# Kernel optimization log

Measured on AMD Instinct MI355X. Metric: run time of the kernel, lower is better.

Reference implementation:

```python
import jax, jax.numpy as jnp
import numpy as np

B, C_LOCAL, C_GUIDE, C2, H, W = 16, 256, 256, 256, 64, 64
MID = C2 // 2          # mlp hidden channels
CQ = C_LOCAL // 4      # offset_gen hidden channels (also = groups)
EPS = 1e-5             # BatchNorm eps (inference mode)


def _conv(x, w, pad=0, groups=1, b=None):
    out = jax.lax.conv_general_dilated(
        x, w, window_strides=(1, 1), padding=((pad, pad), (pad, pad)),
        dimension_numbers=('NCHW', 'OIHW', 'NCHW'), feature_group_count=groups)
    if b is not None:
        out = out + b[None, :, None, None]
    return out


def _bn(x, g, b, m, v):
    scale = g / jnp.sqrt(v + EPS)
    return x * scale[None, :, None, None] + (b - m * scale)[None, :, None, None]


def _grid_sample(img, grid):
    # img: [C,H,W]; grid: [H,W,2] with (x,y) in [-1,1]; bilinear, zeros padding,
    # align_corners=False (pixel = ((g+1)*size - 1)/2)
    C, Hh, Ww = img.shape
    ix = (grid[..., 0] + 1.0) * (Ww * 0.5) - 0.5
    iy = (grid[..., 1] + 1.0) * (Hh * 0.5) - 0.5
    x0 = jnp.floor(ix); y0 = jnp.floor(iy)
    x1 = x0 + 1.0;      y1 = y0 + 1.0
    wx1 = ix - x0; wx0 = 1.0 - wx1
    wy1 = iy - y0; wy0 = 1.0 - wy1

    def gather(xi, yi):
        valid = (xi >= 0) & (xi < Ww) & (yi >= 0) & (yi < Hh)
        xc = jnp.clip(xi, 0, Ww - 1).astype(jnp.int32)
        yc = jnp.clip(yi, 0, Hh - 1).astype(jnp.int32)
        return img[:, yc, xc] * valid.astype(img.dtype)[None]  # [C,H,W]

    return (gather(x0, y0) * (wx0 * wy0)[None]
            + gather(x1, y0) * (wx1 * wy0)[None]
            + gather(x0, y1) * (wx0 * wy1)[None]
            + gather(x1, y1) * (wx1 * wy1)[None])


def setup_inputs() -> dict:
    key = jax.random.key(0)
    ks = jax.random.split(key, 20)
    w = lambda k, s: jax.random.normal(k, s, jnp.float32) * 0.05
    return {
        'x_local': jax.random.normal(ks[0], (B, C_LOCAL, H, W), jnp.float32),
        'x_guide': jax.random.normal(ks[1], (B, C_GUIDE, H, W), jnp.float32),
        'w_align': w(ks[2], (C2, C_GUIDE, 1, 1)),
        'bn1_g': 1.0 + 0.1 * jax.random.normal(ks[3], (C2,), jnp.float32),
        'bn1_b': 0.1 * jax.random.normal(ks[4], (C2,), jnp.float32),
        'bn1_m': 0.1 * jax.random.normal(ks[5], (C2,), jnp.float32),
        'bn1_v': 0.5 + jax.random.uniform(ks[6], (C2,), jnp.float32),
        'w_off1': w(ks[7], (CQ, 4, 3, 3)),   # grouped: in-ch per group = C_LOCAL/CQ = 4
        'w_off2': w(ks[8], (2, CQ, 1, 1)),
        'b_off2': 0.1 * jax.random.normal(ks[9], (2,), jnp.float32),
        'w_mlp1': w(ks[10], (MID, C_LOCAL, 1, 1)),
        'bn2_g': 1.0 + 0.1 * jax.random.normal(ks[11], (MID,), jnp.float32),
        'bn2_b': 0.1 * jax.random.normal(ks[12], (MID,), jnp.float32),
        'bn2_m': 0.1 * jax.random.normal(ks[13], (MID,), jnp.float32),
        'bn2_v': 0.5 + jax.random.uniform(ks[14], (MID,), jnp.float32),
        'w_mlp2': w(ks[15], (C2, MID, 1, 1)),
    }


def reference(x_local, x_guide, w_align, bn1_g, bn1_b, bn1_m, bn1_v,
              w_off1, w_off2, b_off2, w_mlp1, bn2_g, bn2_b, bn2_m, bn2_v,
              w_mlp2):
    # align(x_guide): 1x1 conv + BN
    g = _bn(_conv(x_guide, w_align), bn1_g, bn1_b, bn1_m, bn1_v)
    # offset_gen(x_local): grouped 3x3 conv -> SiLU -> 1x1 conv (bias) -> [B,2,H,W]
    off = _conv(x_local, w_off1, pad=1, groups=CQ)
    off = _conv(jax.nn.silu(off), w_off2, b=b_off2)
    # base grid in [-1,1], (x,y) last
    ys = jnp.linspace(-1.0, 1.0, H)
    xs = jnp.linspace(-1.0, 1.0, W)
    gy, gx = jnp.meshgrid(ys, xs, indexing='ij')
    base = jnp.stack((gx, gy), axis=-1)                      # [H,W,2]
    v_grid = base[None] + off.transpose(0, 2, 3, 1) * (2.0 / max(H, W))
    g_aligned = jax.vmap(_grid_sample)(g, v_grid)            # [B,C2,H,W]
    # mlp(x_local): 1x1 conv -> BN -> GELU(exact) -> 1x1 conv
    l = _conv(x_local, w_mlp1)
    l = jax.nn.gelu(_bn(l, bn2_g, bn2_b, bn2_m, bn2_v), approximate=False)
    l = _conv(l, w_mlp2)
    return jax.nn.silu(g_aligned + l)
```

## Files before the change

### kernel.cpp

```cpp
#include <hip/hip_runtime.h>

typedef unsigned short u16;
typedef unsigned int u32;
typedef __bf16 bf16x8 __attribute__((ext_vector_type(8)));
typedef float f32x4 __attribute__((ext_vector_type(4)));
typedef u16 u16x4 __attribute__((ext_vector_type(4)));
typedef u16 u16x8 __attribute__((ext_vector_type(8)));

#define EPS 1e-5f

__device__ __forceinline__ u16 f2bf(float f) {
  unsigned u = __builtin_bit_cast(unsigned, f);
  u += 0x7FFFu + ((u >> 16) & 1u);
  return (u16)(u >> 16);
}
__device__ __forceinline__ float bf2f(u16 h) {
  unsigned u = ((unsigned)h) << 16;
  return __builtin_bit_cast(float, u);
}

__global__ void prep_weights(
    const float* __restrict__ wa, const float* __restrict__ g1, const float* __restrict__ b1,
    const float* __restrict__ m1, const float* __restrict__ v1,
    const float* __restrict__ w1, const float* __restrict__ g2, const float* __restrict__ b2,
    const float* __restrict__ m2, const float* __restrict__ v2,
    const float* __restrict__ w2,
    u16* __restrict__ Acat, u16* __restrict__ w1_o,
    float* __restrict__ bias1, float* __restrict__ bias2) {
  int c = blockIdx.x, k = threadIdx.x;
  float s1 = g1[c] / sqrtf(v1[c] + EPS);
  if (k < 256) Acat[c * 384 + k] = f2bf(wa[c * 256 + k] * s1);
  else         Acat[c * 384 + k] = f2bf(w2[c * 128 + (k - 256)]);
  if (c < 128) {
    float s2 = g2[c] / sqrtf(v2[c] + EPS);
    if (k < 256) w1_o[c * 256 + k] = f2bf(w1[c * 256 + k] * s2);
    if (k == 256) bias2[c] = b2[c] - m2[c] * s2;
  }
  if (k == 0) bias1[c] = b1[c] - m1[c] * s1;
}

__global__ __launch_bounds__(256) void gconv_kernel(
    const float* __restrict__ xl, const float* __restrict__ w1,
    u16* __restrict__ sbuf) {
  __shared__ float tile[4][18][68];
  const int tid = threadIdx.x;
  const int band = blockIdx.x;
  const int q = blockIdx.y;
  const int b = blockIdx.z;
  const float* xb = xl + ((size_t)b * 256 + 4 * q) * 4096;

  if (tid < 72) {
    int ci0 = tid / 18, r0_ = tid - ci0 * 18;
    float* rowp = &tile[ci0][r0_][0];
    rowp[0] = 0.f; rowp[65] = 0.f; rowp[66] = 0.f; rowp[67] = 0.f;
  }

  const int ci = tid >> 6, col = tid & 63;
  const int gy0 = band * 16 - 1;
  const float* cp = xb + (size_t)ci * 4096 + col;
  float v[18];
#pragma unroll
  for (int r = 0; r < 18; ++r) {
    int gy = gy0 + r;
    int gyc = min(max(gy, 0), 63);
    float raw = cp[gyc * 64];
    v[r] = ((unsigned)gy < 64u) ? raw : 0.f;
  }
#pragma unroll
  for (int r = 0; r < 18; ++r) tile[ci][r][col + 1] = v[r];

  float wq[36];
#pragma unroll
  for (int i = 0; i < 36; ++i) wq[i] = w1[q * 36 + i];
  __syncthreads();

  const int qx = tid & 15, ry = tid >> 4;
  float a0 = 0.f, a1 = 0.f, a2 = 0.f, a3 = 0.f;
#pragma unroll
  for (int ci2 = 0; ci2 < 4; ++ci2) {
#pragma unroll
    for (int dy = 0; dy < 3; ++dy) {
      const float* rowp = &tile[ci2][ry + dy][qx * 4];
      f32x4 m = *(const f32x4*)rowp;
      float2 e = *(const float2*)(rowp + 4);
      float w0 = wq[ci2 * 9 + dy * 3 + 0];
      float w1_ = wq[ci2 * 9 + dy * 3 + 1];
      float w2_ = wq[ci2 * 9 + dy * 3 + 2];
      a0 += w0 * m[0] + w1_ * m[1] + w2_ * m[2];
      a1 += w0 * m[1] + w1_ * m[2] + w2_ * m[3];
      a2 += w0 * m[2] + w1_ * m[3] + w2_ * e.x;
      a3 += w0 * m[3] + w1_ * e.x  + w2_ * e.y;
    }
  }
  u16x4 o;
  o[0] = f2bf(a0 / (1.f + __expf(-a0)));
  o[1] = f2bf(a1 / (1.f + __expf(-a1)));
  o[2] = f2bf(a2 / (1.f + __expf(-a2)));
  o[3] = f2bf(a3 / (1.f + __expf(-a3)));
  u16* sp = sbuf + ((size_t)(b * 64 + q)) * 4096 + (band * 16 + ry) * 64 + qx * 4;
  *(u16x4*)sp = o;
}

__global__ __launch_bounds__(256) void coords_kernel(
    const u16* __restrict__ sbuf, const float* __restrict__ w2,
    const float* __restrict__ b2, float* __restrict__ coords,
    float* __restrict__ wsum) {
  __shared__ float sw2[128];
  const int tid = threadIdx.x;
  if (tid < 128) sw2[tid] = w2[tid];
  __syncthreads();
  const int b = blockIdx.y;
  const int p = blockIdx.x * 256 + tid;
  const u16* sp = sbuf + (size_t)b * 64 * 4096 + p;
  float ax = 0.f, ay = 0.f;
#pragma unroll 8
  for (int q = 0; q < 64; ++q) {
    float v = bf2f(sp[(size_t)q * 4096]);
    ax += sw2[q] * v;
    ay += sw2[64 + q] * v;
  }
  int y = p >> 6, x = p & 63;
  float ix = (64.f / 63.f) * (float)x + ax + b2[0] - 0.5f;
  float iy = (64.f / 63.f) * (float)y + ay + b2[1] - 0.5f;
  ((float2*)coords)[(size_t)b * 4096 + p] = make_float2(ix, iy);
  float x0f = floorf(ix), y0f = floorf(iy);
  int x0 = (int)x0f, y0 = (int)y0f;
  float wx1 = ix - x0f, wx0 = 1.f - wx1;
  float wy1 = iy - y0f, wy0 = 1.f - wy1;
  bool vx0 = (unsigned)x0 < 64u, vx1 = (unsigned)(x0 + 1) < 64u;
  bool vy0 = (unsigned)y0 < 64u, vy1 = (unsigned)(y0 + 1) < 64u;
  float s = (vx0 && vy0 ? wx0 * wy0 : 0.f) + (vx1 && vy0 ? wx1 * wy0 : 0.f) +
            (vx0 && vy1 ? wx0 * wy1 : 0.f) + (vx1 && vy1 ? wx1 * wy1 : 0.f);
  wsum[(size_t)b * 4096 + p] = s;
}

__global__ __launch_bounds__(256, 1) void sampler_kernel(
    const float* __restrict__ xg, const float* __restrict__ coords,
    u16* __restrict__ xh) {
  __shared__ u16 t[64 * 72];
  const int wg = blockIdx.x;
  const int id = (wg & 7) * 512 + (wg >> 3);
  const int kq = id >> 10;
  const int b = (id >> 6) & 15, row = id & 63;
  const int tid = threadIdx.x;
  const int px = tid & 63, ko = tid >> 6;
  const int p = row * 64 + px;
  float2 cd = ((const float2*)coords)[(size_t)b * 4096 + p];
  float ix = cd.x, iy = cd.y;
  float x0f = floorf(ix), y0f = floorf(iy);
  int x0 = (int)x0f, y0 = (int)y0f;
  float wx1 = ix - x0f, wx0 = 1.f - wx1;
  float wy1 = iy - y0f, wy0 = 1.f - wy1;
  bool vx0 = (unsigned)x0 < 64u, vx1 = (unsigned)(x0 + 1) < 64u;
  bool vy0 = (unsigned)y0 < 64u, vy1 = (unsigned)(y0 + 1) < 64u;
  int x0c = min(max(x0, 0), 63), x1c = min(max(x0 + 1, 0), 63);
  int y0c = min(max(y0, 0), 63), y1c = min(max(y0 + 1, 0), 63);
  float w00 = (vx0 && vy0) ? wx0 * wy0 : 0.f;
  float w10 = (vx1 && vy0) ? wx1 * wy0 : 0.f;
  float w01 = (vx0 && vy1) ? wx0 * wy1 : 0.f;
  float w11 = (vx1 && vy1) ? wx1 * wy1 : 0.f;
  const int i00 = y0c * 64 + x0c, i10 = y0c * 64 + x1c;
  const int i01 = y1c * 64 + x0c, i11 = y1c * 64 + x1c;
  const float* bb = xg + ((size_t)b * 256 + kq * 64 + ko * 16) * 4096;

  float v00[16], v10[16], v01[16], v11[16];
#pragma unroll
  for (int kk = 0; kk < 16; ++kk) {
    const float* bp = bb + (size_t)kk * 4096;
    v00[kk] = bp[i00];
    v10[kk] = bp[i10];
    v01[kk] = bp[i01];
    v11[kk] = bp[i11];
  }
  u16 o[16];
#pragma unroll
  for (int kk = 0; kk < 16; ++kk) {
    float v = w00 * v00[kk] + w10 * v10[kk] + w01 * v01[kk] + w11 * v11[kk];
    o[kk] = f2bf(v);
  }
  *(u16x8*)&t[px * 72 + ko * 16] = *(u16x8*)&o[0];
  *(u16x8*)&t[px * 72 + ko * 16 + 8] = *(u16x8*)&o[8];
  __syncthreads();
  const int seg = tid & 7, pxa = tid >> 3;
  u16* base = xh + ((size_t)b * 4096 + row * 64) * 384 + kq * 64 + seg * 8;
#pragma unroll
  for (int h = 0; h < 2; ++h) {
    int pp = pxa + h * 32;
    *(u16x8*)(base + (size_t)pp * 384) = *(const u16x8*)&t[pp * 72 + seg * 8];
  }
}

__global__ __launch_bounds__(256, 2) void gemm_h(
    const u16* __restrict__ A, const float* __restrict__ Bsrc,
    u16* __restrict__ xh, const float* __restrict__ bias) {
  __shared__ u16 Al[2][128][40];
  __shared__ u16 Bl[2][128][40];
  const int tid = threadIdx.x;
  const int b = blockIdx.y;
  const int n0 = blockIdx.x * 128;
  const int wave = tid >> 6, lane = tid & 63;
  const int wr = wave >> 1, wc = wave & 1;
  const int lr = lane & 15, kg = lane >> 4;
  f32x4 acc[4][4] = {};
  const float* Bf = Bsrc + (size_t)b * 256 * 4096;

  const int am = tid >> 1, apos = (tid & 1) * 16;
  const int nq = tid & 31, kq = tid >> 5;
  const int nb = n0 + nq * 4;

  u16x8 qa0, qa1;
  f32x4 qb[4];
  {
    qa0 = *(const u16x8*)(A + (size_t)am * 256 + 0 + apos);
    qa1 = *(const u16x8*)(A + (size_t)am * 256 + 0 + apos + 8);
#pragma unroll
    for (int i = 0; i < 4; ++i)
      qb[i] = *(const f32x4*)(Bf + (size_t)(kq * 4 + i) * 4096 + nb);
  }
  int cur = 0;
  for (int kt = 0; kt < 8; ++kt) {
    *(u16x8*)&Al[cur][am][apos] = qa0;
    *(u16x8*)&Al[cur][am][apos + 8] = qa1;
#pragma unroll
    for (int j = 0; j < 4; ++j) {
      u16x4 w = {f2bf(qb[0][j]), f2bf(qb[1][j]), f2bf(qb[2][j]), f2bf(qb[3][j])};
      *(u16x4*)&Bl[cur][nq * 4 + j][kq * 4] = w;
    }
    if (kt < 7) {
      int k1 = (kt + 1) * 32;
      qa0 = *(const u16x8*)(A + (size_t)am * 256 + k1 + apos);
      qa1 = *(const u16x8*)(A + (size_t)am * 256 + k1 + apos + 8);
#pragma unroll
      for (int i = 0; i < 4; ++i)
        qb[i] = *(const f32x4*)(Bf + (size_t)(k1 + kq * 4 + i) * 4096 + nb);
    }
    __syncthreads();
    bf16x8 af[4], bfr[4];
#pragma unroll
    for (int i = 0; i < 4; ++i) {
      af[i] = *(const bf16x8*)&Al[cur][wr * 64 + i * 16 + lr][kg * 8];
      bfr[i] = *(const bf16x8*)&Bl[cur][wc * 64 + i * 16 + lr][kg * 8];
    }
#pragma unroll
    for (int i = 0; i < 4; ++i)
#pragma unroll
      for (int j = 0; j < 4; ++j)
        acc[i][j] = __builtin_amdgcn_mfma_f32_16x16x32_bf16(af[i], bfr[j], acc[i][j], 0, 0, 0);
    cur ^= 1;
  }
  u16* O = xh + (size_t)b * 4096 * 384 + 256;
#pragma unroll
  for (int i = 0; i < 4; ++i) {
    int rb = wr * 64 + i * 16 + kg * 4;
    f32x4 b4 = *(const f32x4*)(bias + rb);
#pragma unroll
    for (int j = 0; j < 4; ++j) {
      int col = n0 + wc * 64 + j * 16 + lr;
      u16x4 w;
#pragma unroll
      for (int e = 0; e < 4; ++e) {
        float v = acc[i][j][e] + b4[e];
        v = 0.5f * v * (1.f + erff(v * 0.70710678118f));
        w[e] = f2bf(v);
      }
      *(u16x4*)(O + (size_t)col * 384 + rb) = w;
    }
  }
}

__global__ __launch_bounds__(256) void gemm_final(
    const u16* __restrict__ A,
    const u16* __restrict__ xh,
    const float* __restrict__ bias1, const float* __restrict__ wsum,
    float* __restrict__ out) {
  __shared__ __attribute__((aligned(16))) u16 Al[2][128][40];
  __shared__ u16 Bl[2][128][40];
  const int tid = threadIdx.x;
  const int wg = blockIdx.y * 64 + blockIdx.x;
  const int nmb = (wg & 7) * 128 + (wg >> 3);
  const int m = nmb & 1;
  const int n0 = ((nmb >> 1) & 31) * 128;
  const int b = nmb >> 6;
  const int wave = tid >> 6, lane = tid & 63;
  const int wr = wave >> 1, wc = wave & 1;
  const int lr = lane & 15, kg = lane >> 4;
  f32x4 acc[4][4] = {};
  const u16* Ab = A + (size_t)m * 128 * 384;
  const u16* Bb = xh + ((size_t)b * 4096 + n0) * 384;

  const int r0 = tid >> 2, pos0 = (tid & 3) * 8;
  const int r1 = (tid + 256) >> 2, pos1 = pos0;

  u16x8 pa0, pa1, pb0, pb1;
  {
    pa0 = *(const u16x8*)(Ab + (size_t)r0 * 384 + 0 + pos0);
    pb0 = *(const u16x8*)(Bb + (size_t)r0 * 384 + 0 + pos0);
    pa1 = *(const u16x8*)(Ab + (size_t)r1 * 384 + 0 + pos1);
    pb1 = *(const u16x8*)(Bb + (size_t)r1 * 384 + 0 + pos1);
  }
  int cur = 0;
  for (int kt = 0; kt < 12; ++kt) {
    *(u16x8*)&Al[cur][r0][pos0] = pa0;
    *(u16x8*)&Bl[cur][r0][pos0] = pb0;
    *(u16x8*)&Al[cur][r1][pos1] = pa1;
    *(u16x8*)&Bl[cur][r1][pos1] = pb1;
    if (kt < 11) {
      int k1 = (kt + 1) * 32;
      pa0 = *(const u16x8*)(Ab + (size_t)r0 * 384 + k1 + pos0);
      pb0 = *(const u16x8*)(Bb + (size_t)r0 * 384 + k1 + pos0);
      pa1 = *(const u16x8*)(Ab + (size_t)r1 * 384 + k1 + pos1);
      pb1 = *(const u16x8*)(Bb + (size_t)r1 * 384 + k1 + pos1);
    }
    __syncthreads();
    bf16x8 af[4], bfr[4];
#pragma unroll
    for (int i = 0; i < 4; ++i) {
      af[i] = *(const bf16x8*)&Al[cur][wr * 64 + i * 16 + lr][kg * 8];
      bfr[i] = *(const bf16x8*)&Bl[cur][wc * 64 + i * 16 + lr][kg * 8];
    }
#pragma unroll
    for (int i = 0; i < 4; ++i)
#pragma unroll
      for (int j = 0; j < 4; ++j)
        acc[i][j] = __builtin_amdgcn_mfma_f32_16x16x32_bf16(af[i], bfr[j], acc[i][j], 0, 0, 0);
    cur ^= 1;
  }

  float* rep = (float*)&Al[0][0][0];
  float* Ob = out + (size_t)b * 256 * 4096;
  float wsv[4];
#pragma unroll
  for (int j = 0; j < 4; ++j)
    wsv[j] = wsum[(size_t)b * 4096 + n0 + wc * 64 + j * 16 + lr];

#pragma unroll
  for (int i = 0; i < 4; ++i) {
    __syncthreads();
    f32x4 b4 = *(const f32x4*)(bias1 + m * 128 + wr * 64 + i * 16 + kg * 4);
#pragma unroll
    for (int j = 0; j < 4; ++j) {
#pragma unroll
      for (int e = 0; e < 4; ++e) {
        float v = acc[i][j][e] + b4[e] * wsv[j];
        v = v / (1.f + __expf(-v));
        rep[(wr * 16 + kg * 4 + e) * 132 + wc * 64 + j * 16 + lr] = v;
      }
    }
    __syncthreads();
#pragma unroll
    for (int pass = 0; pass < 4; ++pass) {
      int lr_ = pass * 8 + (tid >> 5);
      int lc_ = (tid & 31) * 4;
      f32x4 v4 = *(const f32x4*)&rep[lr_ * 132 + lc_];
      int grow = m * 128 + (lr_ >> 4) * 64 + i * 16 + (lr_ & 15);
      *(f32x4*)&Ob[(size_t)grow * 4096 + n0 + lc_] = v4;
    }
  }
}

extern "C" void kernel_launch(void* const* d_in, const int* in_sizes, int n_in,
                              void* d_out, int out_size, void* d_ws, size_t ws_size,
                              hipStream_t stream) {
  const float* x_local = (const float*)d_in[0];
  const float* x_guide = (const float*)d_in[1];
  const float* w_align = (const float*)d_in[2];
  const float* bn1_g = (const float*)d_in[3];
  const float* bn1_b = (const float*)d_in[4];
  const float* bn1_m = (const float*)d_in[5];
  const float* bn1_v = (const float*)d_in[6];
  const float* w_off1 = (const float*)d_in[7];
  const float* w_off2 = (const float*)d_in[8];
  const float* b_off2 = (const float*)d_in[9];
  const float* w_mlp1 = (const float*)d_in[10];
  const float* bn2_g = (const float*)d_in[11];
  const float* bn2_b = (const float*)d_in[12];
  const float* bn2_m = (const float*)d_in[13];
  const float* bn2_v = (const float*)d_in[14];
  const float* w_mlp2 = (const float*)d_in[15];

  char* ws = (char*)d_ws;
  u16* Acat = (u16*)(ws + 0);
  u16* w1_bf = (u16*)(ws + 196608);
  float* bias1 = (float*)(ws + 262144);
  float* bias2 = (float*)(ws + 263168);
  float* wsum = (float*)(ws + 263680);
  float* coords = (float*)(ws + 525824);
  u16* xh = (u16*)(ws + 1050112);
  u16* sbuf = xh;

  prep_weights<<<256, 384, 0, stream>>>(
      w_align, bn1_g, bn1_b, bn1_m, bn1_v,
      w_mlp1, bn2_g, bn2_b, bn2_m, bn2_v, w_mlp2,
      Acat, w1_bf, bias1, bias2);

  gconv_kernel<<<dim3(4, 64, 16), 256, 0, stream>>>(x_local, w_off1, sbuf);

  coords_kernel<<<dim3(16, 16), 256, 0, stream>>>(sbuf, w_off2, b_off2, coords, wsum);

  sampler_kernel<<<4096, 256, 0, stream>>>(x_guide, coords, xh);

  gemm_h<<<dim3(32, 16), 256, 0, stream>>>(w1_bf, x_local, xh, bias2);

  gemm_final<<<dim3(64, 16), 256, 0, stream>>>(Acat, xh, bias1, wsum, (float*)d_out);
}
```

Baseline: 108.9 us.

## Merge grouped conv and MLP GEMM into one heterogeneous launch

Combines the grouped 3x3 conv kernel and the first MLP GEMM into a single kernel of 4608 blocks. Every 9th block runs the GEMM tile and the other eight run conv bands, so both independent stages share the GPU concurrently. The conv scratch buffer moves into the output buffer, since it previously aliased xh, which the GEMM now writes at the same time. This saves one launch and overlaps compute-bound GEMM work with memory-bound conv work, at the cost of a larger LDS footprint and higher register pressure for the conv blocks.

```diff
diff --git a/kernel.cpp b/kernel.cpp
--- a/kernel.cpp
+++ b/kernel.cpp
@@ -39,66 +39,147 @@
   if (k == 0) bias1[c] = b1[c] - m1[c] * s1;
 }
 
-__global__ __launch_bounds__(256) void gconv_kernel(
-    const float* __restrict__ xl, const float* __restrict__ w1,
-    u16* __restrict__ sbuf) {
-  __shared__ float tile[4][18][68];
+__global__ __launch_bounds__(256, 2) void fat_kernel(
+    const float* __restrict__ xl, const float* __restrict__ w1g,
+    u16* __restrict__ sbuf,
+    const u16* __restrict__ A, u16* __restrict__ xh,
+    const float* __restrict__ bias) {
+  __shared__ __attribute__((aligned(16))) char lds[40960];
   const int tid = threadIdx.x;
-  const int band = blockIdx.x;
-  const int q = blockIdx.y;
-  const int b = blockIdx.z;
-  const float* xb = xl + ((size_t)b * 256 + 4 * q) * 4096;
-
-  if (tid < 72) {
-    int ci0 = tid / 18, r0_ = tid - ci0 * 18;
-    float* rowp = &tile[ci0][r0_][0];
-    rowp[0] = 0.f; rowp[65] = 0.f; rowp[66] = 0.f; rowp[67] = 0.f;
-  }
-
-  const int ci = tid >> 6, col = tid & 63;
-  const int gy0 = band * 16 - 1;
-  const float* cp = xb + (size_t)ci * 4096 + col;
-  float v[18];
-#pragma unroll
-  for (int r = 0; r < 18; ++r) {
-    int gy = gy0 + r;
-    int gyc = min(max(gy, 0), 63);
-    float raw = cp[gyc * 64];
-    v[r] = ((unsigned)gy < 64u) ? raw : 0.f;
-  }
-#pragma unroll
-  for (int r = 0; r < 18; ++r) tile[ci][r][col + 1] = v[r];
-
-  float wq[36];
-#pragma unroll
-  for (int i = 0; i < 36; ++i) wq[i] = w1[q * 36 + i];
-  __syncthreads();
-
-  const int qx = tid & 15, ry = tid >> 4;
-  float a0 = 0.f, a1 = 0.f, a2 = 0.f, a3 = 0.f;
-#pragma unroll
-  for (int ci2 = 0; ci2 < 4; ++ci2) {
-#pragma unroll
-    for (int dy = 0; dy < 3; ++dy) {
-      const float* rowp = &tile[ci2][ry + dy][qx * 4];
-      f32x4 m = *(const f32x4*)rowp;
-      float2 e = *(const float2*)(rowp + 4);
-      float w0 = wq[ci2 * 9 + dy * 3 + 0];
-      float w1_ = wq[ci2 * 9 + dy * 3 + 1];
-      float w2_ = wq[ci2 * 9 + dy * 3 + 2];
-      a0 += w0 * m[0] + w1_ * m[1] + w2_ * m[2];
-      a1 += w0 * m[1] + w1_ * m[2] + w2_ * m[3];
-      a2 += w0 * m[2] + w1_ * m[3] + w2_ * e.x;
-      a3 += w0 * m[3] + w1_ * e.x  + w2_ * e.y;
-    }
-  }
-  u16x4 o;
-  o[0] = f2bf(a0 / (1.f + __expf(-a0)));
-  o[1] = f2bf(a1 / (1.f + __expf(-a1)));
-  o[2] = f2bf(a2 / (1.f + __expf(-a2)));
-  o[3] = f2bf(a3 / (1.f + __expf(-a3)));
-  u16* sp = sbuf + ((size_t)(b * 64 + q)) * 4096 + (band * 16 + ry) * 64 + qx * 4;
-  *(u16x4*)sp = o;
+  const int bid = blockIdx.x;
+  const int grp = bid / 9;
+  const int slot = bid - grp * 9;
+
+  if (slot == 4) {
+    u16 (*Al)[128][40] = (u16(*)[128][40])lds;
+    u16 (*Bl)[128][40] = (u16(*)[128][40])(lds + 20480);
+    const int b = grp >> 5;
+    const int n0 = (grp & 31) * 128;
+    const int wave = tid >> 6, lane = tid & 63;
+    const int wr = wave >> 1, wc = wave & 1;
+    const int lr = lane & 15, kg = lane >> 4;
+    f32x4 acc[4][4] = {};
+    const float* Bf = xl + (size_t)b * 256 * 4096;
+
+    const int am = tid >> 1, apos = (tid & 1) * 16;
+    const int nq = tid & 31, kq = tid >> 5;
+    const int nb = n0 + nq * 4;
+
+    u16x8 qa0, qa1;
+    f32x4 qb[4];
+    {
+      qa0 = *(const u16x8*)(A + (size_t)am * 256 + 0 + apos);
+      qa1 = *(const u16x8*)(A + (size_t)am * 256 + 0 + apos + 8);
+#pragma unroll
+      for (int i = 0; i < 4; ++i)
+        qb[i] = *(const f32x4*)(Bf + (size_t)(kq * 4 + i) * 4096 + nb);
+    }
+    int cur = 0;
+    for (int kt = 0; kt < 8; ++kt) {
+      *(u16x8*)&Al[cur][am][apos] = qa0;
+      *(u16x8*)&Al[cur][am][apos + 8] = qa1;
+#pragma unroll
+      for (int j = 0; j < 4; ++j) {
+        u16x4 w = {f2bf(qb[0][j]), f2bf(qb[1][j]), f2bf(qb[2][j]), f2bf(qb[3][j])};
+        *(u16x4*)&Bl[cur][nq * 4 + j][kq * 4] = w;
+      }
+      if (kt < 7) {
+        int k1 = (kt + 1) * 32;
+        qa0 = *(const u16x8*)(A + (size_t)am * 256 + k1 + apos);
+        qa1 = *(const u16x8*)(A + (size_t)am * 256 + k1 + apos + 8);
+#pragma unroll
+        for (int i = 0; i < 4; ++i)
+          qb[i] = *(const f32x4*)(Bf + (size_t)(k1 + kq * 4 + i) * 4096 + nb);
+      }
+      __syncthreads();
+      bf16x8 af[4], bfr[4];
+#pragma unroll
+      for (int i = 0; i < 4; ++i) {
+        af[i] = *(const bf16x8*)&Al[cur][wr * 64 + i * 16 + lr][kg * 8];
+        bfr[i] = *(const bf16x8*)&Bl[cur][wc * 64 + i * 16 + lr][kg * 8];
+      }
+#pragma unroll
+      for (int i = 0; i < 4; ++i)
+#pragma unroll
+        for (int j = 0; j < 4; ++j)
+          acc[i][j] = __builtin_amdgcn_mfma_f32_16x16x32_bf16(af[i], bfr[j], acc[i][j], 0, 0, 0);
+      cur ^= 1;
+    }
+    u16* O = xh + (size_t)b * 4096 * 384 + 256;
+#pragma unroll
+    for (int i = 0; i < 4; ++i) {
+      int rb = wr * 64 + i * 16 + kg * 4;
+      f32x4 b4 = *(const f32x4*)(bias + rb);
+#pragma unroll
+      for (int j = 0; j < 4; ++j) {
+        int col = n0 + wc * 64 + j * 16 + lr;
+        u16x4 w;
+#pragma unroll
+        for (int e = 0; e < 4; ++e) {
+          float v = acc[i][j][e] + b4[e];
+          v = 0.5f * v * (1.f + erff(v * 0.70710678118f));
+          w[e] = f2bf(v);
+        }
+        *(u16x4*)(O + (size_t)col * 384 + rb) = w;
+      }
+    }
+  } else {
+    float (*tile)[18][68] = (float(*)[18][68])lds;
+    const int idx = grp * 8 + (slot < 4 ? slot : slot - 1);
+    const int band = idx & 3, q = (idx >> 2) & 63, b = idx >> 8;
+    const float* xb = xl + ((size_t)b * 256 + 4 * q) * 4096;
+
+    if (tid < 72) {
+      int ci0 = tid / 18, r0_ = tid - ci0 * 18;
+      float* rowp = &tile[ci0][r0_][0];
+      rowp[0] = 0.f; rowp[65] = 0.f; rowp[66] = 0.f; rowp[67] = 0.f;
+    }
+
+    const int ci = tid >> 6, col = tid & 63;
+    const int gy0 = band * 16 - 1;
+    const float* cp = xb + (size_t)ci * 4096 + col;
+    float v[18];
+#pragma unroll
+    for (int r = 0; r < 18; ++r) {
+      int gy = gy0 + r;
+      int gyc = min(max(gy, 0), 63);
+      float raw = cp[gyc * 64];
+      v[r] = ((unsigned)gy < 64u) ? raw : 0.f;
+    }
+#pragma unroll
+    for (int r = 0; r < 18; ++r) tile[ci][r][col + 1] = v[r];
+
+    float wq[36];
+#pragma unroll
+    for (int i = 0; i < 36; ++i) wq[i] = w1g[q * 36 + i];
+    __syncthreads();
+
+    const int qx = tid & 15, ry = tid >> 4;
+    float a0 = 0.f, a1 = 0.f, a2 = 0.f, a3 = 0.f;
+#pragma unroll
+    for (int ci2 = 0; ci2 < 4; ++ci2) {
+#pragma unroll
+      for (int dy = 0; dy < 3; ++dy) {
+        const float* rowp = &tile[ci2][ry + dy][qx * 4];
+        f32x4 m = *(const f32x4*)rowp;
+        float2 e = *(const float2*)(rowp + 4);
+        float w0 = wq[ci2 * 9 + dy * 3 + 0];
+        float w1_ = wq[ci2 * 9 + dy * 3 + 1];
+        float w2_ = wq[ci2 * 9 + dy * 3 + 2];
+        a0 += w0 * m[0] + w1_ * m[1] + w2_ * m[2];
+        a1 += w0 * m[1] + w1_ * m[2] + w2_ * m[3];
+        a2 += w0 * m[2] + w1_ * m[3] + w2_ * e.x;
+        a3 += w0 * m[3] + w1_ * e.x  + w2_ * e.y;
+      }
+    }
+    u16x4 o;
+    o[0] = f2bf(a0 / (1.f + __expf(-a0)));
+    o[1] = f2bf(a1 / (1.f + __expf(-a1)));
+    o[2] = f2bf(a2 / (1.f + __expf(-a2)));
+    o[3] = f2bf(a3 / (1.f + __expf(-a3)));
+    u16* sp = sbuf + ((size_t)(b * 64 + q)) * 4096 + (band * 16 + ry) * 64 + qx * 4;
+    *(u16x4*)sp = o;
+  }
 }
 
 __global__ __launch_bounds__(256) void coords_kernel(
@@ -190,84 +271,6 @@
   }
 }
 
-__global__ __launch_bounds__(256, 2) void gemm_h(
-    const u16* __restrict__ A, const float* __restrict__ Bsrc,
-    u16* __restrict__ xh, const float* __restrict__ bias) {
-  __shared__ u16 Al[2][128][40];
-  __shared__ u16 Bl[2][128][40];
-  const int tid = threadIdx.x;
-  const int b = blockIdx.y;
-  const int n0 = blockIdx.x * 128;
-  const int wave = tid >> 6, lane = tid & 63;
-  const int wr = wave >> 1, wc = wave & 1;
-  const int lr = lane & 15, kg = lane >> 4;
-  f32x4 acc[4][4] = {};
-  const float* Bf = Bsrc + (size_t)b * 256 * 4096;
-
-  const int am = tid >> 1, apos = (tid & 1) * 16;
-  const int nq = tid & 31, kq = tid >> 5;
-  const int nb = n0 + nq * 4;
-
-  u16x8 qa0, qa1;
-  f32x4 qb[4];
-  {
-    qa0 = *(const u16x8*)(A + (size_t)am * 256 + 0 + apos);
-    qa1 = *(const u16x8*)(A + (size_t)am * 256 + 0 + apos + 8);
-#pragma unroll
-    for (int i = 0; i < 4; ++i)
-      qb[i] = *(const f32x4*)(Bf + (size_t)(kq * 4 + i) * 4096 + nb);
-  }
-  int cur = 0;
-  for (int kt = 0; kt < 8; ++kt) {
-    *(u16x8*)&Al[cur][am][apos] = qa0;
-    *(u16x8*)&Al[cur][am][apos + 8] = qa1;
-#pragma unroll
-    for (int j = 0; j < 4; ++j) {
-      u16x4 w = {f2bf(qb[0][j]), f2bf(qb[1][j]), f2bf(qb[2][j]), f2bf(qb[3][j])};
-      *(u16x4*)&Bl[cur][nq * 4 + j][kq * 4] = w;
-    }
-    if (kt < 7) {
-      int k1 = (kt + 1) * 32;
-      qa0 = *(const u16x8*)(A + (size_t)am * 256 + k1 + apos);
-      qa1 = *(const u16x8*)(A + (size_t)am * 256 + k1 + apos + 8);
-#pragma unroll
-      for (int i = 0; i < 4; ++i)
-        qb[i] = *(const f32x4*)(Bf + (size_t)(k1 + kq * 4 + i) * 4096 + nb);
-    }
-    __syncthreads();
-    bf16x8 af[4], bfr[4];
-#pragma unroll
-    for (int i = 0; i < 4; ++i) {
-      af[i] = *(const bf16x8*)&Al[cur][wr * 64 + i * 16 + lr][kg * 8];
-      bfr[i] = *(const bf16x8*)&Bl[cur][wc * 64 + i * 16 + lr][kg * 8];
-    }
-#pragma unroll
-    for (int i = 0; i < 4; ++i)
-#pragma unroll
-      for (int j = 0; j < 4; ++j)
-        acc[i][j] = __builtin_amdgcn_mfma_f32_16x16x32_bf16(af[i], bfr[j], acc[i][j], 0, 0, 0);
-    cur ^= 1;
-  }
-  u16* O = xh + (size_t)b * 4096 * 384 + 256;
-#pragma unroll
-  for (int i = 0; i < 4; ++i) {
-    int rb = wr * 64 + i * 16 + kg * 4;
-    f32x4 b4 = *(const f32x4*)(bias + rb);
-#pragma unroll
-    for (int j = 0; j < 4; ++j) {
-      int col = n0 + wc * 64 + j * 16 + lr;
-      u16x4 w;
-#pragma unroll
-      for (int e = 0; e < 4; ++e) {
-        float v = acc[i][j][e] + b4[e];
-        v = 0.5f * v * (1.f + erff(v * 0.70710678118f));
-        w[e] = f2bf(v);
-      }
-      *(u16x4*)(O + (size_t)col * 384 + rb) = w;
-    }
-  }
-}
-
 __global__ __launch_bounds__(256) void gemm_final(
     const u16* __restrict__ A,
     const u16* __restrict__ xh,
@@ -386,20 +389,19 @@
   float* wsum = (float*)(ws + 263680);
   float* coords = (float*)(ws + 525824);
   u16* xh = (u16*)(ws + 1050112);
-  u16* sbuf = xh;
+  u16* sbuf = (u16*)d_out;
 
   prep_weights<<<256, 384, 0, stream>>>(
       w_align, bn1_g, bn1_b, bn1_m, bn1_v,
       w_mlp1, bn2_g, bn2_b, bn2_m, bn2_v, w_mlp2,
       Acat, w1_bf, bias1, bias2);
 
-  gconv_kernel<<<dim3(4, 64, 16), 256, 0, stream>>>(x_local, w_off1, sbuf);
+  fat_kernel<<<4608, 256, 0, stream>>>(
+      x_local, w_off1, sbuf, w1_bf, xh, bias2);
 
   coords_kernel<<<dim3(16, 16), 256, 0, stream>>>(sbuf, w_off2, b_off2, coords, wsum);
 
   sampler_kernel<<<4096, 256, 0, stream>>>(x_guide, coords, xh);
 
-  gemm_h<<<dim3(32, 16), 256, 0, stream>>>(w1_bf, x_local, xh, bias2);
-
   gemm_final<<<dim3(64, 16), 256, 0, stream>>>(Acat, xh, bias1, wsum, (float*)d_out);
 }
```

Result: slower. 112.4 us (+3.3%).
